# Performance work log

Hardware: AMD Instinct MI355X
Metric: run time of the kernel (lower is better)

## Reference

```python
import jax, jax.numpy as jnp
import numpy as np

B, C_IN, H, W = 32, 64, 64, 64
D, O, S_SP, K = 256, 512, 4, 3


def setup_inputs() -> dict:
    key = jax.random.key(0)
    k1, k2, k3, k4, k5 = jax.random.split(key, 5)
    x = jax.random.normal(k1, (B, C_IN, H, W), dtype=jnp.float32)
    dictionary = jax.random.normal(k2, (D, C_IN, K, K), dtype=jnp.float32)
    lookup_coefficients = jax.random.normal(k3, (O, S_SP), dtype=jnp.float32)
    bias = jax.random.normal(k4, (O,), dtype=jnp.float32)
    lookup_indices = jax.random.randint(k5, (O, S_SP), 0, D)
    return {
        "x": x,
        "dictionary": dictionary,
        "lookup_coefficients": lookup_coefficients,
        "bias": bias,
        "lookup_indices": lookup_indices,
    }


def reference(x, dictionary, lookup_coefficients, bias, lookup_indices):
    # Dictionary conv: S has shape [B, D, H, W] (stride 1, padding 1, 3x3 kernel)
    S = jax.lax.conv_general_dilated(
        x, dictionary,
        window_strides=(1, 1),
        padding=((1, 1), (1, 1)),
        dimension_numbers=("NCHW", "OIHW", "NCHW"),
    )
    # Build dense [O, D] combine matrix via scatter-add (duplicate indices
    # accumulate, matching the original += loop), then one GEMM.
    rows = jnp.arange(O)[:, None]  # [O, 1] broadcast against [O, sparsity]
    Wc = jnp.zeros((O, D), dtype=S.dtype).at[rows, lookup_indices].add(lookup_coefficients)
    out = jnp.einsum("bdhw,od->bohw", S, Wc)
    return out + bias[None, :, None, None]
```

## Files before the change

### kernel.cpp

```cpp
#include <hip/hip_runtime.h>
#include <stdint.h>

#define NB 32
#define NC 64
#define NH 64
#define NW 64
#define NO 512
#define HP 66

typedef __bf16 bf16x8 __attribute__((ext_vector_type(8)));
typedef short  s16x8  __attribute__((ext_vector_type(8)));
typedef float  f32x4  __attribute__((ext_vector_type(4)));

__device__ __forceinline__ uint16_t f2bf(float f) {
  uint32_t u = __builtin_bit_cast(uint32_t, f);
  u += 0x7fffu + ((u >> 16) & 1u);
  return (uint16_t)(u >> 16);
}

__device__ __forceinline__ void gld16(const uint16_t* g, uint16_t* l) {
  __builtin_amdgcn_global_load_lds(
      (const __attribute__((address_space(1))) void*)(g),
      (__attribute__((address_space(3))) void*)(l), 16, 0, 0);
}

__global__ void k_build_w(const float* __restrict__ dict,
                          const float* __restrict__ coef,
                          const int*   __restrict__ idx,
                          uint16_t*    __restrict__ Wl) {
  __shared__ float tmp[576];
  const int o = blockIdx.x;
  const int t = threadIdx.x;
  float v = 0.f;
#pragma unroll
  for (int s = 0; s < 4; ++s)
    v += coef[o * 4 + s] * dict[idx[o * 4 + s] * 576 + t];
  tmp[t] = v;
  __syncthreads();
  const int c = t & 63, p = t >> 6;
  const int sl = ((p * NO + o) * 8 + ((c >> 3) ^ (o & 7))) * 8 + (c & 7);
  Wl[sl] = f2bf(tmp[c * 9 + p]);
}

__global__ void k_nhwc(const float* __restrict__ x, uint16_t* __restrict__ xh) {
  const int bh = blockIdx.x;
  const int b = bh / HP, hp = bh % HP;
  const int t = threadIdx.x;
  uint16_t* row = xh + (size_t)(b * HP + hp) * 4096;
  if (hp == 0 || hp == HP - 1) {
    int4* r4 = reinterpret_cast<int4*>(row);
    r4[t]       = int4{0, 0, 0, 0};
    r4[t + 256] = int4{0, 0, 0, 0};
    return;
  }
  __shared__ float tile[64][65];
  const int h = hp - 1;
  const int w = t & 63;
#pragma unroll
  for (int c = (t >> 6); c < 64; c += 4)
    tile[c][w] = x[((size_t)(b * NC + c) * NH + h) * NW + w];
  __syncthreads();
#pragma unroll
  for (int i = 0; i < 2; ++i) {
    const int s = t + i * 256;
    const int w2 = s >> 3, cb = s & 7;
    uint32_t d[4];
#pragma unroll
    for (int j = 0; j < 4; ++j) {
      const uint32_t lo = f2bf(tile[cb * 8 + 2 * j][w2]);
      const uint32_t hi = f2bf(tile[cb * 8 + 2 * j + 1][w2]);
      d[j] = lo | (hi << 16);
    }
    reinterpret_cast<int4*>(row)[w2 * 8 + (cb ^ (w2 & 7))] =
        int4{(int)d[0], (int)d[1], (int)d[2], (int)d[3]};
  }
}

__global__ __launch_bounds__(256, 2) void k_conv(
    const uint16_t* __restrict__ xh,
    const uint16_t* __restrict__ Wl,
    const float*    __restrict__ bias,
    float*          __restrict__ out) {
  __shared__ __align__(16) uint16_t xs[4 * 66 * 64];
  __shared__ __align__(16) uint16_t as[2 * 128 * 64];

  const int t = threadIdx.x;
  const int flat = blockIdx.x;
  const int s    = (flat & 7) * 512 + (flat >> 3);
  const int ot   = s & 3;
  const int gy   = s >> 2;
  const int o0 = ot * 128;
  const int b  = gy >> 5;
  const int h0 = (gy & 31) * 2;

  const int lane = t & 63;
  const int wid  = t >> 6;

  if (t < 64) {
    const int r = t >> 4, side = (t >> 3) & 1, k = t & 7;
    reinterpret_cast<int4*>(xs)[r * 528 + side * 520 + k] = int4{0, 0, 0, 0};
  }
  {
    const uint16_t* src = xh + (size_t)(b * HP + h0 + wid) * 4096;
    uint16_t* dst = xs + wid * 4224 + 64;
#pragma unroll
    for (int k = 0; k < 8; ++k)
      gld16(src + k * 512 + lane * 8, dst + k * 512);
  }
  {
    const uint16_t* src = Wl + o0 * 64;
#pragma unroll
    for (int j = 0; j < 4; ++j) {
      const int ch = wid * 4 + j;
      gld16(src + ch * 512 + lane * 8, as + ch * 512);
    }
  }

  const int wm  = wid >> 1;
  const int wn  = wid & 1;
  const int l15 = lane & 15;
  const int g   = lane >> 4;

  f32x4 acc[4][4] = {};

  __syncthreads();

#pragma unroll
  for (int p = 0; p < 9; ++p) {
    const int buf = p & 1;
    if (p < 8) {
      const uint16_t* src = Wl + (p + 1) * 32768 + o0 * 64;
      uint16_t* dst = as + (buf ^ 1) * 8192;
#pragma unroll
      for (int j = 0; j < 4; ++j) {
        const int ch = wid * 4 + j;
        gld16(src + ch * 512 + lane * 8, dst + ch * 512);
      }
    }

    const int dh = p / 3 - 1, dw = p % 3 - 1;
    const int rbase = (wn + dh + 1) * 4224;
    const uint16_t* asb = as + buf * 8192;

#pragma unroll
    for (int q = 0; q < 2; ++q) {
      bf16x8 af[4], bfr[4];
#pragma unroll
      for (int m = 0; m < 4; ++m) {
        const int orow = wm * 64 + m * 16 + l15;
        const int cb = (q * 4 + g) ^ (orow & 7);
        af[m] = __builtin_bit_cast(bf16x8,
            *reinterpret_cast<const s16x8*>(asb + orow * 64 + cb * 8));
      }
#pragma unroll
      for (int n = 0; n < 4; ++n) {
        const int wv = n * 16 + l15 + dw;
        const int cb = (q * 4 + g) ^ (wv & 7);
        bfr[n] = __builtin_bit_cast(bf16x8,
            *reinterpret_cast<const s16x8*>(xs + rbase + (wv + 1) * 64 + cb * 8));
      }
#pragma unroll
      for (int m = 0; m < 4; ++m)
#pragma unroll
        for (int n = 0; n < 4; ++n)
          acc[m][n] = __builtin_amdgcn_mfma_f32_16x16x32_bf16(
              af[m], bfr[n], acc[m][n], 0, 0, 0);
    }
    __syncthreads();
  }

  const int hpix = h0 + wn;
#pragma unroll
  for (int m = 0; m < 4; ++m) {
#pragma unroll
    for (int rr = 0; rr < 4; ++rr) {
      const int o = o0 + wm * 64 + m * 16 + g * 4 + rr;
      const float bv = bias[o];
      float* orow_p = out + ((size_t)(b * NO + o) * NH + hpix) * NW;
#pragma unroll
      for (int n = 0; n < 4; ++n)
        orow_p[n * 16 + l15] = acc[m][n][rr] + bv;
    }
  }
}

extern "C" void kernel_launch(void* const* d_in, const int* in_sizes, int n_in,
                              void* d_out, int out_size, void* d_ws, size_t ws_size,
                              hipStream_t stream) {
  const float* x    = (const float*)d_in[0];
  const float* dict = (const float*)d_in[1];
  const float* coef = (const float*)d_in[2];
  const float* bias = (const float*)d_in[3];
  const int*   idx  = (const int*)d_in[4];
  float* out = (float*)d_out;

  uint16_t* xh = (uint16_t*)d_ws;
  uint16_t* Wl = (uint16_t*)((char*)d_ws + (18u << 20));

  hipLaunchKernelGGL(k_build_w, dim3(NO), dim3(576), 0, stream, dict, coef, idx, Wl);
  hipLaunchKernelGGL(k_nhwc, dim3(NB * HP), dim3(256), 0, stream, x, xh);
  hipLaunchKernelGGL(k_conv, dim3(4096), dim3(256), 0, stream, xh, Wl, bias, out);
}
```

Before: 115.6 us.

## Enlarge conv tile to eight output rows with triple-buffered weight pipeline

Each block now covers 8 output rows (10 padded input rows) with 512 threads and a 4x8 MFMA accumulator per wave. This reuses each staged weight tile across more pixels and cuts the grid from 4096 to 1024 blocks. Weight staging becomes a three-buffer ring with explicit vmcnt waits and a raw barrier in place of __syncthreads, and s_setprio is raised around the MFMA bursts. The larger LDS footprint (about 132KB) and doubled accumulators raise register and LDS pressure, which may limit occupancy.

```diff
diff --git a/kernel.cpp b/kernel.cpp
--- a/kernel.cpp
+++ b/kernel.cpp
@@ -76,75 +76,83 @@
   }
 }
 
-__global__ __launch_bounds__(256, 2) void k_conv(
+__global__ __launch_bounds__(512, 2) void k_conv(
     const uint16_t* __restrict__ xh,
     const uint16_t* __restrict__ Wl,
     const float*    __restrict__ bias,
     float*          __restrict__ out) {
-  __shared__ __align__(16) uint16_t xs[4 * 66 * 64];
-  __shared__ __align__(16) uint16_t as[2 * 128 * 64];
+  __shared__ __align__(16) uint16_t xs[10 * 66 * 64];
+  __shared__ __align__(16) uint16_t as[3 * 128 * 64];
 
   const int t = threadIdx.x;
   const int flat = blockIdx.x;
-  const int s    = (flat & 7) * 512 + (flat >> 3);
+  const int s    = (flat & 7) * 128 + (flat >> 3);
   const int ot   = s & 3;
   const int gy   = s >> 2;
   const int o0 = ot * 128;
-  const int b  = gy >> 5;
-  const int h0 = (gy & 31) * 2;
+  const int b  = gy >> 3;
+  const int h0 = (gy & 7) * 8;
 
   const int lane = t & 63;
   const int wid  = t >> 6;
 
-  if (t < 64) {
-    const int r = t >> 4, side = (t >> 3) & 1, k = t & 7;
-    reinterpret_cast<int4*>(xs)[r * 528 + side * 520 + k] = int4{0, 0, 0, 0};
-  }
+  if (t < 160) {
+    const int r = t >> 4, sl = (t >> 3) & 1, j = t & 7;
+    reinterpret_cast<int4*>(xs)[r * 528 + sl * 520 + j] = int4{0, 0, 0, 0};
+  }
+
   {
-    const uint16_t* src = xh + (size_t)(b * HP + h0 + wid) * 4096;
-    uint16_t* dst = xs + wid * 4224 + 64;
+    const uint16_t* srow = xh + (size_t)(b * HP + h0 + wid) * 4096;
+    uint16_t* drow = xs + wid * 4224 + 64;
 #pragma unroll
     for (int k = 0; k < 8; ++k)
-      gld16(src + k * 512 + lane * 8, dst + k * 512);
-  }
-  {
-    const uint16_t* src = Wl + o0 * 64;
-#pragma unroll
-    for (int j = 0; j < 4; ++j) {
-      const int ch = wid * 4 + j;
-      gld16(src + ch * 512 + lane * 8, as + ch * 512);
-    }
-  }
-
-  const int wm  = wid >> 1;
-  const int wn  = wid & 1;
+      gld16(srow + k * 512 + lane * 8, drow + k * 512);
+    const int r2 = 8 + (wid >> 2);
+    const int kb = (wid & 3) * 2;
+    const uint16_t* srow2 = xh + (size_t)(b * HP + h0 + r2) * 4096;
+    uint16_t* drow2 = xs + r2 * 4224 + 64;
+    gld16(srow2 + kb * 512 + lane * 8, drow2 + kb * 512);
+    gld16(srow2 + (kb + 1) * 512 + lane * 8, drow2 + (kb + 1) * 512);
+  }
+  asm volatile("" ::: "memory");
+
+  auto stage_a = [&](int p, int bufsel) {
+    const uint16_t* src = Wl + (size_t)p * 32768 + o0 * 64;
+    uint16_t* dst = as + bufsel * 8192;
+#pragma unroll
+    for (int j = 0; j < 2; ++j) {
+      const int ch = wid * 2 + j;
+      gld16(src + ch * 512 + lane * 8, dst + ch * 512);
+    }
+  };
+  stage_a(0, 0);
+  asm volatile("" ::: "memory");
+  stage_a(1, 1);
+  asm volatile("" ::: "memory");
+
+  const int wm  = wid & 1;
+  const int wn  = wid >> 1;
   const int l15 = lane & 15;
   const int g   = lane >> 4;
 
-  f32x4 acc[4][4] = {};
-
-  __syncthreads();
+  f32x4 acc[4][8] = {};
 
 #pragma unroll
   for (int p = 0; p < 9; ++p) {
-    const int buf = p & 1;
-    if (p < 8) {
-      const uint16_t* src = Wl + (p + 1) * 32768 + o0 * 64;
-      uint16_t* dst = as + (buf ^ 1) * 8192;
-#pragma unroll
-      for (int j = 0; j < 4; ++j) {
-        const int ch = wid * 4 + j;
-        gld16(src + ch * 512 + lane * 8, dst + ch * 512);
-      }
-    }
+    if (p == 0)      asm volatile("s_waitcnt vmcnt(2) lgkmcnt(0)" ::: "memory");
+    else if (p == 8) asm volatile("s_waitcnt vmcnt(0)" ::: "memory");
+    else             asm volatile("s_waitcnt vmcnt(2)" ::: "memory");
+    __builtin_amdgcn_s_barrier();
+    asm volatile("" ::: "memory");
+
+    if (p + 2 <= 8) stage_a(p + 2, (p + 2) % 3);
 
     const int dh = p / 3 - 1, dw = p % 3 - 1;
-    const int rbase = (wn + dh + 1) * 4224;
-    const uint16_t* asb = as + buf * 8192;
+    const uint16_t* asb = as + (p % 3) * 8192;
 
 #pragma unroll
     for (int q = 0; q < 2; ++q) {
-      bf16x8 af[4], bfr[4];
+      bf16x8 af[4], bfr[8];
 #pragma unroll
       for (int m = 0; m < 4; ++m) {
         const int orow = wm * 64 + m * 16 + l15;
@@ -153,33 +161,35 @@
             *reinterpret_cast<const s16x8*>(asb + orow * 64 + cb * 8));
       }
 #pragma unroll
-      for (int n = 0; n < 4; ++n) {
-        const int wv = n * 16 + l15 + dw;
-        const int cb = (q * 4 + g) ^ (wv & 7);
+      for (int n = 0; n < 8; ++n) {
+        const int row = wn * 2 + (n >> 2) + dh + 1;
+        const int wv  = (n & 3) * 16 + l15 + dw;
+        const int cb  = (q * 4 + g) ^ (wv & 7);
         bfr[n] = __builtin_bit_cast(bf16x8,
-            *reinterpret_cast<const s16x8*>(xs + rbase + (wv + 1) * 64 + cb * 8));
+            *reinterpret_cast<const s16x8*>(xs + row * 4224 + (wv + 1) * 64 + cb * 8));
       }
+      __builtin_amdgcn_s_setprio(1);
 #pragma unroll
       for (int m = 0; m < 4; ++m)
 #pragma unroll
-        for (int n = 0; n < 4; ++n)
+        for (int n = 0; n < 8; ++n)
           acc[m][n] = __builtin_amdgcn_mfma_f32_16x16x32_bf16(
               af[m], bfr[n], acc[m][n], 0, 0, 0);
-    }
-    __syncthreads();
-  }
-
-  const int hpix = h0 + wn;
+      __builtin_amdgcn_s_setprio(0);
+    }
+  }
+
+  const int hb = h0 + wn * 2;
 #pragma unroll
   for (int m = 0; m < 4; ++m) {
 #pragma unroll
     for (int rr = 0; rr < 4; ++rr) {
       const int o = o0 + wm * 64 + m * 16 + g * 4 + rr;
       const float bv = bias[o];
-      float* orow_p = out + ((size_t)(b * NO + o) * NH + hpix) * NW;
-#pragma unroll
-      for (int n = 0; n < 4; ++n)
-        orow_p[n * 16 + l15] = acc[m][n][rr] + bv;
+      float* op = out + ((size_t)(b * NO + o) * NH + hb) * NW;
+#pragma unroll
+      for (int n = 0; n < 8; ++n)
+        op[(n >> 2) * NW + (n & 3) * 16 + l15] = acc[m][n][rr] + bv;
     }
   }
 }
@@ -199,5 +209,5 @@
 
   hipLaunchKernelGGL(k_build_w, dim3(NO), dim3(576), 0, stream, dict, coef, idx, Wl);
   hipLaunchKernelGGL(k_nhwc, dim3(NB * HP), dim3(256), 0, stream, x, xh);
-  hipLaunchKernelGGL(k_conv, dim3(4096), dim3(256), 0, stream, xh, Wl, bias, out);
-}
+  hipLaunchKernelGGL(k_conv, dim3(1024), dim3(512), 0, stream, xh, Wl, bias, out);
+}
```

After: 117.9 us. +2.0%, slower.
